# Optimization experiments

Measured on AMD Instinct MI355X. Metric: run time of the kernel, lower is better.

The kernel has to match this reference:

```python
import jax, jax.numpy as jnp
import numpy as np

N = 10000      # nodes
E = 160000     # edges (avg degree 16)
H = 128        # hidden_dim
L = 4          # propagation_depth
G = 64         # graphs in batch
ATOM_V = 119
BOND_V = 5
AVG_D_LOG = 1.0
EPS_SCALE = 1e-8


def setup_inputs() -> dict:
    key = jax.random.key(0)
    ks = jax.random.split(key, 12)
    x = jax.random.randint(ks[0], (N,), 0, ATOM_V)
    edge_index = jax.random.randint(ks[1], (2, E), 0, N)
    edge_attr = jax.random.randint(ks[2], (E,), 0, BOND_V)
    batch = jnp.sort(jax.random.randint(ks[3], (N,), 0, G))
    atom_emb = jax.random.normal(ks[4], (ATOM_V, H), jnp.float32) * 0.1
    bond_emb = jax.random.normal(ks[5], (BOND_V, H), jnp.float32) * 0.1
    pre_W = jax.random.normal(ks[6], (L, 3 * H, H), jnp.float32) / np.sqrt(3 * H)
    pre_b = jnp.zeros((L, H), jnp.float32)
    post_W = jax.random.normal(ks[7], (L, 10 * H, H), jnp.float32) / np.sqrt(10 * H)
    post_b = jnp.zeros((L, H), jnp.float32)
    out_W1 = jax.random.normal(ks[8], (3 * H, H), jnp.float32) / np.sqrt(3 * H)
    out_b1 = jnp.zeros((H,), jnp.float32)
    out_W2 = jax.random.normal(ks[9], (H, 1), jnp.float32) / np.sqrt(H)
    out_b2 = jnp.zeros((1,), jnp.float32)
    return {"x": x, "edge_index": edge_index, "edge_attr": edge_attr, "batch": batch,
            "atom_emb": atom_emb, "bond_emb": bond_emb,
            "pre_W": pre_W, "pre_b": pre_b, "post_W": post_W, "post_b": post_b,
            "out_W1": out_W1, "out_b1": out_b1, "out_W2": out_W2, "out_b2": out_b2}


def _seg_mean_sum_max(v, idx, num_seg, cnt):
    s = jax.ops.segment_sum(v, idx, num_segments=num_seg)
    mean = s / jnp.maximum(cnt, 1.0)[:, None]
    mx = jax.ops.segment_max(v, idx, num_segments=num_seg)
    mx = jnp.where(cnt[:, None] > 0, mx, 0.0)  # empty segments -> 0 (torch scatter)
    return mean, s, mx


def _clean(a):
    return jnp.where(jnp.isnan(a) | jnp.isinf(a), 0.0, a)


def reference(x, edge_index, edge_attr, batch, atom_emb, bond_emb,
              pre_W, pre_b, post_W, post_b, out_W1, out_b1, out_W2, out_b2):
    h = atom_emb[x]            # [N, H] atom encoder
    e = bond_emb[edge_attr]    # [E, H] bond encoder
    row, col = edge_index[0], edge_index[1]
    n = h.shape[0]
    deg = jax.ops.segment_sum(jnp.ones_like(col, jnp.float32), col, num_segments=n)
    D = deg[:, None]
    logD = jnp.log(D + 1.0)
    amp_fac = logD / AVG_D_LOG                       # amplification scaler
    att_fac = AVG_D_LOG / jnp.maximum(logD, EPS_SCALE)  # attenuation scaler
    n_layers = pre_W.shape[0]
    for l in range(n_layers):
        h_in = h
        z2 = jnp.concatenate([h[row], h[col], e], axis=-1)         # [E, 3H]
        msg = z2 @ pre_W[l] + pre_b[l]                             # pretrans (1 layer, no act)
        mean, s, mx = _seg_mean_sum_max(msg, col, n, deg)
        hagg = jnp.concatenate([mean, s, mx], axis=-1)             # [N, 3H]
        hcat = jnp.concatenate([hagg, hagg * amp_fac, hagg * att_fac, h_in], axis=-1)  # [N, 10H]
        h = hcat @ post_W[l] + post_b[l]                           # posttrans (1 layer)
        h = h + h_in                                               # residual
    # readout over graphs
    cnt = jax.ops.segment_sum(jnp.ones((n,), jnp.float32), batch, num_segments=G)
    rmean, rsum, rmax = _seg_mean_sum_max(h, batch, G, cnt)
    r = _clean(jnp.concatenate([rmean, rsum, rmax], axis=-1))      # [G, 3H]
    out = jax.nn.relu(r @ out_W1 + out_b1) @ out_W2 + out_b2       # [G, 1]
    return _clean(out)
```

## Files before the change

kernel.cpp:

```cpp
#include <hip/hip_runtime.h>
#include <hip/hip_bf16.h>
#include <math.h>

#define NN 10000
#define NE 160000
#define HD 128
#define NL 4
#define NG 64

typedef __attribute__((ext_vector_type(8))) short bf16x8;
typedef __attribute__((ext_vector_type(4))) short bf16x4;
typedef __attribute__((ext_vector_type(4))) float f32x4;

static __device__ __forceinline__ short f2bf(float f) {
    unsigned u = __float_as_uint(f);
    unsigned r = (u + 0x7FFFu + ((u >> 16) & 1u)) >> 16;
    return (short)r;
}
static __device__ __forceinline__ float bf2f(short s) {
    return __uint_as_float(((unsigned)(unsigned short)s) << 16);
}

__global__ void setup1_kernel(const int* __restrict__ x, const float* __restrict__ atom_emb,
                              float* __restrict__ h, float* __restrict__ deg,
                              int* __restrict__ cursor) {
    int idx = blockIdx.x * 256 + threadIdx.x;
    if (idx < NN) { deg[idx] = 0.f; cursor[idx] = 0; }
    if (idx < NN * HD) {
        int n = idx >> 7, f = idx & 127;
        h[idx] = atom_emb[x[n] * HD + f];
    }
}

__global__ __launch_bounds__(256) void setup2_kernel(
    const int* __restrict__ col, float* __restrict__ deg,
    const float* __restrict__ bond_emb,
    const float* __restrict__ pre_W, const float* __restrict__ pre_b,
    const float* __restrict__ post_W,
    float* __restrict__ btab, short* __restrict__ pre_Wt, short* __restrict__ post_Wt) {
    int b = blockIdx.x;
    if (b < 625) {
        int e = b * 256 + threadIdx.x;
        if (e < NE) atomicAdd(&deg[col[e]], 1.f);
        return;
    }
    if (b < 645) {
        int lb = b - 625;
        if (threadIdx.x < 128) {
            int l = lb / 5, bb = lb % 5;
            int f = threadIdx.x;
            const float* W2 = pre_W + (size_t)l * 384 * HD + 256 * HD;
            const float* eb = bond_emb + bb * HD;
            float acc = pre_b[l * HD + f];
            for (int k = 0; k < HD; ++k) acc = fmaf(eb[k], W2[k * HD + f], acc);
            btab[(l * 5 + bb) * HD + f] = acc;
        }
        return;
    }
    int idx = (b - 645) * 256 + threadIdx.x;
    if (idx < NL * 4 * 256 * 32) {
        int l = idx >> 15;
        int r = idx & 32767;
        int kblk = r >> 13;
        int rr = r & 8191;
        int j = rr >> 5, k = rr & 31;
        const float* Wl = pre_W + (size_t)l * 384 * HD;
        float v = (j < 128) ? Wl[(kblk * 32 + k) * HD + j]
                            : Wl[(128 + kblk * 32 + k) * HD + (j - 128)];
        pre_Wt[idx] = f2bf(v);
    }
    if (idx < NL * 40 * 128 * 32) {
        int l = idx / 163840;
        int r = idx % 163840;
        int kblk = r >> 12;
        int rr = r & 4095;
        int j = rr >> 5, k = rr & 31;
        post_Wt[idx] = f2bf(post_W[(size_t)l * 163840 + (size_t)(kblk * 32 + k) * HD + j]);
    }
}

__global__ __launch_bounds__(1024) void scan_facs_kernel(const float* __restrict__ deg,
                                                         int* __restrict__ offsets,
                                                         float* __restrict__ amp,
                                                         float* __restrict__ att) {
    __shared__ int s[1024];
    int t = threadIdx.x;
    int base = t * 10;
    int v[10];
    int lsum = 0;
    #pragma unroll
    for (int i = 0; i < 10; ++i) {
        int idx = base + i;
        int d = (idx < NN) ? (int)deg[idx] : 0;
        v[i] = d;
        lsum += d;
        if (idx < NN) {
            float logD = logf((float)d + 1.f);
            amp[idx] = logD;
            att[idx] = 1.f / fmaxf(logD, 1e-8f);
        }
    }
    s[t] = lsum;
    __syncthreads();
    for (int off = 1; off < 1024; off <<= 1) {
        int x2 = (t >= off) ? s[t - off] : 0;
        __syncthreads();
        s[t] += x2;
        __syncthreads();
    }
    int run = s[t] - lsum;
    #pragma unroll
    for (int i = 0; i < 10; ++i) {
        int idx = base + i;
        if (idx < NN) offsets[idx] = run;
        run += v[i];
    }
    if (t == 1023) offsets[NN] = run;
}

__global__ void scatter_kernel(const int* __restrict__ row, const int* __restrict__ col,
                               const int* __restrict__ ea, const int* __restrict__ offsets,
                               int* __restrict__ cursor, int* __restrict__ perm) {
    int e = blockIdx.x * 256 + threadIdx.x;
    if (e < NE) {
        int c = col[e];
        int pos = offsets[c] + atomicAdd(&cursor[c], 1);
        perm[pos] = row[e] | (ea[e] << 14);
    }
}

__global__ __launch_bounds__(256) void pre_gemm_mfma(const float* __restrict__ h,
                                                     const short* __restrict__ Wt,
                                                     short* __restrict__ hw0,
                                                     float* __restrict__ hw1) {
    __shared__ short Ap[16][136];
    int t = threadIdx.x;
    int nb = blockIdx.x * 16;
    {
        int nl = t >> 4, f = (t & 15) * 8;
        int n = nb + nl;
        const float* src = h + (size_t)n * HD + f;
        float4 x0 = *(const float4*)src, x1 = *(const float4*)(src + 4);
        bf16x8 pk;
        pk[0]=f2bf(x0.x); pk[1]=f2bf(x0.y); pk[2]=f2bf(x0.z); pk[3]=f2bf(x0.w);
        pk[4]=f2bf(x1.x); pk[5]=f2bf(x1.y); pk[6]=f2bf(x1.z); pk[7]=f2bf(x1.w);
        *(bf16x8*)&Ap[nl][f] = pk;
    }
    __syncthreads();
    int wave = t >> 6, lane = t & 63;
    int lx = lane & 15, kb = lane >> 4;
    f32x4 acc[4];
    #pragma unroll
    for (int j = 0; j < 4; ++j) acc[j] = (f32x4){0.f, 0.f, 0.f, 0.f};

    for (int ks = 0; ks < 4; ++ks) {
        bf16x8 a = *(const bf16x8*)&Ap[lx][ks * 32 + kb * 8];
        const short* bp = Wt + (size_t)ks * 8192 + (size_t)(wave * 64 + lx) * 32 + kb * 8;
        #pragma unroll
        for (int jj = 0; jj < 4; ++jj) {
            bf16x8 bfr = *(const bf16x8*)(bp + jj * 512);
            acc[jj] = __builtin_amdgcn_mfma_f32_16x16x32_bf16(a, bfr, acc[jj], 0, 0, 0);
        }
    }
    #pragma unroll
    for (int jj = 0; jj < 4; ++jj) {
        int c = wave * 64 + jj * 16 + lx;
        #pragma unroll
        for (int r_ = 0; r_ < 4; ++r_) {
            int n2 = nb + kb * 4 + r_;
            if (c < 128) hw0[(size_t)n2 * HD + c] = f2bf(acc[jj][r_]);
            else         hw1[(size_t)n2 * HD + (c - 128)] = acc[jj][r_];
        }
    }
}

__global__ __launch_bounds__(256) void agg_node_gemm_mfma(
    const short* __restrict__ hw0, const float* __restrict__ hw1,
    const float* __restrict__ btab,
    const int* __restrict__ offsets, const int* __restrict__ perm,
    const float* __restrict__ hin,
    const float* __restrict__ amp, const float* __restrict__ att,
    const short* __restrict__ Wt , const float* __restrict__ bias,
    float* __restrict__ hout,
    const short* __restrict__ nextWt ,
    short* __restrict__ hw0n, float* __restrict__ hw1n) {
    __shared__ short Ap[16][1288];
    __shared__ short Ap2[16][136];
    __shared__ float btab_s[5][128];
    int t = threadIdx.x;
    int nb = blockIdx.x * 16;

    if (t < 160) {
        int b = t >> 5, f4 = (t & 31) * 4;
        *(f32x4*)&btab_s[b][f4] = *(const f32x4*)(btab + b * HD + f4);
    }
    __syncthreads();

    {
        int nl = t >> 4;
        int n = nb + nl;
        int f = (t & 15) * 8;
        int s0 = offsets[n];
        int d = offsets[n + 1] - s0;
        f32x4 sum0 = {0.f,0.f,0.f,0.f}, sum1 = {0.f,0.f,0.f,0.f};
        f32x4 mx0 = {-INFINITY,-INFINITY,-INFINITY,-INFINITY};
        f32x4 mx1 = mx0;
        int i = 0;
        for (; i + 2 <= d; i += 2) {
            int p0 = perm[s0 + i], p1 = perm[s0 + i + 1];
            bf16x8 a0 = *(const bf16x8*)(hw0 + (size_t)(p0 & 16383) * HD + f);
            bf16x8 a1 = *(const bf16x8*)(hw0 + (size_t)(p1 & 16383) * HD + f);
            const float* t0 = &btab_s[p0 >> 14][f];
            const float* t1 = &btab_s[p1 >> 14][f];
            f32x4 b00 = *(const f32x4*)t0, b01 = *(const f32x4*)(t0 + 4);
            f32x4 b10 = *(const f32x4*)t1, b11 = *(const f32x4*)(t1 + 4);
            f32x4 v00, v01, v10, v11;
            #pragma unroll
            for (int q = 0; q < 4; ++q) {
                v00[q] = bf2f(a0[q]) + b00[q];
                v01[q] = bf2f(a0[q + 4]) + b01[q];
                v10[q] = bf2f(a1[q]) + b10[q];
                v11[q] = bf2f(a1[q + 4]) + b11[q];
            }
            sum0 += v00 + v10; sum1 += v01 + v11;
            #pragma unroll
            for (int q = 0; q < 4; ++q) {
                mx0[q] = fmaxf(mx0[q], fmaxf(v00[q], v10[q]));
                mx1[q] = fmaxf(mx1[q], fmaxf(v01[q], v11[q]));
            }
        }
        if (i < d) {
            int p0 = perm[s0 + i];
            bf16x8 a0 = *(const bf16x8*)(hw0 + (size_t)(p0 & 16383) * HD + f);
            const float* t0 = &btab_s[p0 >> 14][f];
            f32x4 b00 = *(const f32x4*)t0, b01 = *(const f32x4*)(t0 + 4);
            f32x4 v00, v01;
            #pragma unroll
            for (int q = 0; q < 4; ++q) {
                v00[q] = bf2f(a0[q]) + b00[q];
                v01[q] = bf2f(a0[q + 4]) + b01[q];
            }
            sum0 += v00; sum1 += v01;
            #pragma unroll
            for (int q = 0; q < 4; ++q) {
                mx0[q] = fmaxf(mx0[q], v00[q]);
                mx1[q] = fmaxf(mx1[q], v01[q]);
            }
        }
        const float* cp = hw1 + (size_t)n * HD + f;
        f32x4 c0 = *(const f32x4*)cp, c1 = *(const f32x4*)(cp + 4);
        f32x4 me0, me1, so0, so1, mo0, mo1;
        if (d > 0) {
            float df = (float)d, di = 1.f / df;
            so0 = sum0 + df * c0;  so1 = sum1 + df * c1;
            me0 = sum0 * di + c0;  me1 = sum1 * di + c1;
            mo0 = mx0 + c0;        mo1 = mx1 + c1;
        } else {
            me0 = (f32x4){0.f,0.f,0.f,0.f}; me1 = me0;
            so0 = me0; so1 = me0; mo0 = me0; mo1 = me0;
        }
        float f_amp = amp[n], f_att = att[n];
        #pragma unroll
        for (int fi = 0; fi < 3; ++fi) {
            float fac = (fi == 0) ? 1.f : ((fi == 1) ? f_amp : f_att);
            #pragma unroll
            for (int ag = 0; ag < 3; ++ag) {
                f32x4 r0 = (ag == 0) ? me0 : ((ag == 1) ? so0 : mo0);
                f32x4 r1 = (ag == 0) ? me1 : ((ag == 1) ? so1 : mo1);
                bf16x8 pk;
                #pragma unroll
                for (int q = 0; q < 4; ++q) {
                    pk[q]     = f2bf(r0[q] * fac);
                    pk[q + 4] = f2bf(r1[q] * fac);
                }
                *(bf16x8*)&Ap[nl][(fi * 3 + ag) * 128 + f] = pk;
            }
        }
        {
            const float* src = hin + (size_t)n * HD + f;
            float4 x0 = *(const float4*)src, x1 = *(const float4*)(src + 4);
            bf16x8 pk;
            pk[0]=f2bf(x0.x); pk[1]=f2bf(x0.y); pk[2]=f2bf(x0.z); pk[3]=f2bf(x0.w);
            pk[4]=f2bf(x1.x); pk[5]=f2bf(x1.y); pk[6]=f2bf(x1.z); pk[7]=f2bf(x1.w);
            *(bf16x8*)&Ap[nl][9 * 128 + f] = pk;
        }
    }
    __syncthreads();

    int wave = t >> 6, lane = t & 63;
    int lx = lane & 15, kb = lane >> 4;
    f32x4 acc0 = {0.f,0.f,0.f,0.f}, acc1 = acc0;
    for (int ks = 0; ks < 40; ++ks) {
        bf16x8 a = *(const bf16x8*)&Ap[lx][ks * 32 + kb * 8];
        const short* bp = Wt + (size_t)ks * 4096 + (size_t)(wave * 32 + lx) * 32 + kb * 8;
        bf16x8 b0 = *(const bf16x8*)bp;
        bf16x8 b1 = *(const bf16x8*)(bp + 512);
        acc0 = __builtin_amdgcn_mfma_f32_16x16x32_bf16(a, b0, acc0, 0, 0, 0);
        acc1 = __builtin_amdgcn_mfma_f32_16x16x32_bf16(a, b1, acc1, 0, 0, 0);
    }
    #pragma unroll
    for (int jj = 0; jj < 2; ++jj) {
        int c = wave * 32 + jj * 16 + lx;
        float bc = bias[c];
        f32x4 av = jj ? acc1 : acc0;
        #pragma unroll
        for (int r_ = 0; r_ < 4; ++r_) {
            int n2 = nb + kb * 4 + r_;
            size_t off = (size_t)n2 * HD + c;
            float ho = av[r_] + bc + hin[off];
            hout[off] = ho;
            Ap2[n2 - nb][c] = f2bf(ho);
        }
    }
    if (nextWt == nullptr) return;
    __syncthreads();

    f32x4 acc[4];
    #pragma unroll
    for (int j = 0; j < 4; ++j) acc[j] = (f32x4){0.f, 0.f, 0.f, 0.f};
    for (int ks = 0; ks < 4; ++ks) {
        bf16x8 a = *(const bf16x8*)&Ap2[lx][ks * 32 + kb * 8];
        const short* bp = nextWt + (size_t)ks * 8192 + (size_t)(wave * 64 + lx) * 32 + kb * 8;
        #pragma unroll
        for (int jj = 0; jj < 4; ++jj) {
            bf16x8 bfr = *(const bf16x8*)(bp + jj * 512);
            acc[jj] = __builtin_amdgcn_mfma_f32_16x16x32_bf16(a, bfr, acc[jj], 0, 0, 0);
        }
    }
    #pragma unroll
    for (int jj = 0; jj < 4; ++jj) {
        int c = wave * 64 + jj * 16 + lx;
        #pragma unroll
        for (int r_ = 0; r_ < 4; ++r_) {
            int n2 = nb + kb * 4 + r_;
            if (c < 128) hw0n[(size_t)n2 * HD + c] = f2bf(acc[jj][r_]);
            else         hw1n[(size_t)n2 * HD + (c - 128)] = acc[jj][r_];
        }
    }
}

__global__ __launch_bounds__(256) void pool_out_kernel(
    const float* __restrict__ h, const int* __restrict__ batch,
    const float* __restrict__ W1, const float* __restrict__ b1,
    const float* __restrict__ W2, const float* __restrict__ b2,
    float* __restrict__ out)
{
    __shared__ float rs[384];
    __shared__ float red[256];
    __shared__ float s2[128], m2[128];
    int g = blockIdx.x, t = threadIdx.x;
    int lo = 0, hi = NN;
    while (lo < hi) { int mid = (lo + hi) >> 1; if (batch[mid] < g) lo = mid + 1; else hi = mid; }
    int lo2 = lo, hi2 = NN;
    while (lo2 < hi2) { int mid = (lo2 + hi2) >> 1; if (batch[mid] < g + 1) lo2 = mid + 1; else hi2 = mid; }
    int cnt = lo2 - lo;
    int f = t & 127, grp = t >> 7;
    float sum = 0.f, mx = -INFINITY;
    for (int n = lo + grp; n < lo2; n += 2) {
        float v = h[(size_t)n * HD + f];
        sum += v; mx = fmaxf(mx, v);
    }
    if (grp == 1) { s2[f] = sum; m2[f] = mx; }
    __syncthreads();
    if (grp == 0) {
        sum += s2[f]; mx = fmaxf(mx, m2[f]);
        float mean = (cnt > 0) ? sum / (float)cnt : 0.f;
        float so = (cnt > 0) ? sum : 0.f;
        float mo = (cnt > 0) ? mx : 0.f;
        if (isnan(mean) || isinf(mean)) mean = 0.f;
        if (isnan(so) || isinf(so)) so = 0.f;
        if (isnan(mo) || isinf(mo)) mo = 0.f;
        rs[f] = mean; rs[128 + f] = so; rs[256 + f] = mo;
    }
    __syncthreads();
    {
        int j = t & 127, kh = t >> 7;
        float acc = 0.f;
        for (int k = kh * 192; k < kh * 192 + 192; ++k)
            acc = fmaf(rs[k], W1[k * HD + j], acc);
        red[t] = acc;
    }
    __syncthreads();
    if (t < 128) {
        float v = fmaxf(red[t] + red[128 + t] + b1[t], 0.f);
        red[t] = v * W2[t];
    }
    __syncthreads();
    for (int s = 64; s > 0; s >>= 1) {
        if (t < s) red[t] += red[t + s];
        __syncthreads();
    }
    if (t == 0) {
        float o = red[0] + b2[0];
        if (isnan(o) || isinf(o)) o = 0.f;
        out[g] = o;
    }
}

extern "C" void kernel_launch(void* const* d_in, const int* in_sizes, int n_in,
                              void* d_out, int out_size, void* d_ws, size_t ws_size,
                              hipStream_t stream)
{
    const int* x          = (const int*)d_in[0];
    const int* ei         = (const int*)d_in[1];
    const int* ea         = (const int*)d_in[2];
    const int* batch      = (const int*)d_in[3];
    const float* atom_emb = (const float*)d_in[4];
    const float* bond_emb = (const float*)d_in[5];
    const float* pre_W    = (const float*)d_in[6];
    const float* pre_b    = (const float*)d_in[7];
    const float* post_W   = (const float*)d_in[8];
    const float* post_b   = (const float*)d_in[9];
    const float* out_W1   = (const float*)d_in[10];
    const float* out_b1   = (const float*)d_in[11];
    const float* out_W2   = (const float*)d_in[12];
    const float* out_b2   = (const float*)d_in[13];
    float* out = (float*)d_out;
    const int* row = ei;
    const int* col = ei + NE;

    char* p = (char*)d_ws;
    auto alloc = [&](size_t bytes) { char* r = p; p += (bytes + 255) & ~(size_t)255; return r; };
    float*    deg     = (float*)alloc((size_t)NN * 4);
    float*    amp     = (float*)alloc((size_t)NN * 4);
    float*    att     = (float*)alloc((size_t)NN * 4);
    int*      offsets = (int*)alloc((size_t)(NN + 1) * 4);
    int*      cursor  = (int*)alloc((size_t)NN * 4);
    int*      perm    = (int*)alloc((size_t)NE * 4);
    float*    hA      = (float*)alloc((size_t)NN * HD * 4);
    float*    hB      = (float*)alloc((size_t)NN * HD * 4);
    short*    hw0A    = (short*)alloc((size_t)NN * HD * 2);
    short*    hw0B    = (short*)alloc((size_t)NN * HD * 2);
    float*    hw1A    = (float*)alloc((size_t)NN * HD * 4);
    float*    hw1B    = (float*)alloc((size_t)NN * HD * 4);
    float*    btab    = (float*)alloc((size_t)NL * 5 * HD * 4);
    short*    pre_Wt  = (short*)alloc((size_t)NL * 4 * 256 * 32 * 2);
    short*    post_Wt = (short*)alloc((size_t)NL * 40 * 128 * 32 * 2);

    setup1_kernel<<<(NN * HD) / 256, 256, 0, stream>>>(x, atom_emb, hA, deg, cursor);
    setup2_kernel<<<645 + (NL * 40 * 128 * 32 + 255) / 256, 256, 0, stream>>>(
        col, deg, bond_emb, pre_W, pre_b, post_W, btab, pre_Wt, post_Wt);
    scan_facs_kernel<<<1, 1024, 0, stream>>>(deg, offsets, amp, att);
    scatter_kernel<<<(NE + 255) / 256, 256, 0, stream>>>(row, col, ea, offsets, cursor, perm);

    pre_gemm_mfma<<<NN / 16, 256, 0, stream>>>(hA, pre_Wt, hw0A, hw1A);

    float* curH = hA;
    float* nxtH = hB;
    for (int l = 0; l < NL; ++l) {
        short* hw0_in  = (l & 1) ? hw0B : hw0A;
        float* hw1_in  = (l & 1) ? hw1B : hw1A;
        short* hw0_out = (l & 1) ? hw0A : hw0B;
        float* hw1_out = (l & 1) ? hw1A : hw1B;
        const short* nextWt = (l + 1 < NL) ? (pre_Wt + (size_t)(l + 1) * 4 * 256 * 32) : nullptr;
        agg_node_gemm_mfma<<<NN / 16, 256, 0, stream>>>(
            hw0_in, hw1_in, btab + (size_t)l * 5 * HD, offsets, perm,
            curH, amp, att, post_Wt + (size_t)l * 40 * 128 * 32,
            post_b + (size_t)l * HD, nxtH, nextWt, hw0_out, hw1_out);
        float* tmp = curH; curH = nxtH; nxtH = tmp;
    }

    pool_out_kernel<<<NG, 256, 0, stream>>>(curH, batch, out_W1, out_b1, out_W2, out_b2, out);
}
```

Baseline: 287.5 us.

## Fuse all stages into one cooperative persistent kernel with grid syncs

Replaces the chain of separate kernel launches (setup, scan, scatter, pre-GEMM, four layer kernels, pooling) with one cooperative kernel of 625 blocks that separates stages with grid.sync, removing per-launch overhead and inter-kernel gaps. The layer kernel also shrinks its shared-memory A tile by storing only the three aggregates in bf16 and applying the amp/att scalers and the h_in conversion on the fly during the MFMA loop, which lowers LDS use to allow more resident blocks. The degree scan now runs in a single 256-thread block inside the grid, and grid-wide barriers add their own sync cost. A multi-kernel fallback is kept when cooperative occupancy is insufficient.

```diff
diff --git a/kernel.cpp b/kernel.cpp
--- a/kernel.cpp
+++ b/kernel.cpp
@@ -1,12 +1,19 @@
 #include <hip/hip_runtime.h>
+#include <hip/hip_cooperative_groups.h>
 #include <hip/hip_bf16.h>
 #include <math.h>
+
+namespace cg = cooperative_groups;
 
 #define NN 10000
 #define NE 160000
 #define HD 128
 #define NL 4
 #define NG 64
+#define NBLK 625
+#define NTHR 256
+#define GRIDTHREADS 160000
+#define SMEM_BYTES 19584
 
 typedef __attribute__((ext_vector_type(8))) short bf16x8;
 typedef __attribute__((ext_vector_type(4))) short bf16x4;
@@ -20,6 +27,272 @@
 static __device__ __forceinline__ float bf2f(short s) {
     return __uint_as_float(((unsigned)(unsigned short)s) << 16);
 }
+
+
+__device__ __forceinline__ void pre_gemm_body(char* smem, int t, int nb,
+        const float* __restrict__ h, const short* __restrict__ Wt,
+        short* __restrict__ hw0, float* __restrict__ hw1) {
+    short (*Ap)[136] = (short(*)[136])smem;
+    {
+        int nl = t >> 4, f = (t & 15) * 8;
+        int n = nb + nl;
+        const float* src = h + (size_t)n * HD + f;
+        float4 x0 = *(const float4*)src, x1 = *(const float4*)(src + 4);
+        bf16x8 pk;
+        pk[0]=f2bf(x0.x); pk[1]=f2bf(x0.y); pk[2]=f2bf(x0.z); pk[3]=f2bf(x0.w);
+        pk[4]=f2bf(x1.x); pk[5]=f2bf(x1.y); pk[6]=f2bf(x1.z); pk[7]=f2bf(x1.w);
+        *(bf16x8*)&Ap[nl][f] = pk;
+    }
+    __syncthreads();
+    int wave = t >> 6, lane = t & 63;
+    int lx = lane & 15, kb = lane >> 4;
+    f32x4 acc[4];
+    #pragma unroll
+    for (int j = 0; j < 4; ++j) acc[j] = (f32x4){0.f, 0.f, 0.f, 0.f};
+    for (int ks = 0; ks < 4; ++ks) {
+        bf16x8 a = *(const bf16x8*)&Ap[lx][ks * 32 + kb * 8];
+        const short* bp = Wt + (size_t)ks * 8192 + (size_t)(wave * 64 + lx) * 32 + kb * 8;
+        #pragma unroll
+        for (int jj = 0; jj < 4; ++jj) {
+            bf16x8 bfr = *(const bf16x8*)(bp + jj * 512);
+            acc[jj] = __builtin_amdgcn_mfma_f32_16x16x32_bf16(a, bfr, acc[jj], 0, 0, 0);
+        }
+    }
+    #pragma unroll
+    for (int jj = 0; jj < 4; ++jj) {
+        int c = wave * 64 + jj * 16 + lx;
+        #pragma unroll
+        for (int r_ = 0; r_ < 4; ++r_) {
+            int n2 = nb + kb * 4 + r_;
+            if (c < 128) hw0[(size_t)n2 * HD + c] = f2bf(acc[jj][r_]);
+            else         hw1[(size_t)n2 * HD + (c - 128)] = acc[jj][r_];
+        }
+    }
+}
+
+__device__ __forceinline__ void fused_layer_body(char* smem, int t, int nb,
+        const short* __restrict__ hw0_in, const float* __restrict__ hw1_in,
+        const float* __restrict__ btabL,
+        const int* __restrict__ offsets, const int* __restrict__ perm,
+        const float* __restrict__ curH,
+        const float* __restrict__ amp, const float* __restrict__ att,
+        const short* __restrict__ Wt , const float* __restrict__ bias,
+        float* __restrict__ nxtH,
+        const short* __restrict__ nextWt, short* __restrict__ hw0o, float* __restrict__ hw1o) {
+    short (*aggB)[3][132] = (short(*)[3][132])smem;
+    float (*btab_s)[128]  = (float(*)[128])(smem + 12672);
+    short (*Ap2)[136]     = (short(*)[136])(smem + 15232);
+
+    if (t < 160) {
+        int bb = t >> 5, f4 = (t & 31) * 4;
+        *(f32x4*)&btab_s[bb][f4] = *(const f32x4*)(btabL + bb * HD + f4);
+    }
+    __syncthreads();
+
+    {
+        int nl = t >> 4;
+        int n = nb + nl;
+        int f = (t & 15) * 8;
+        int s0 = offsets[n];
+        int d = offsets[n + 1] - s0;
+        f32x4 sum0 = {0.f,0.f,0.f,0.f}, sum1 = {0.f,0.f,0.f,0.f};
+        f32x4 mx0 = {-INFINITY,-INFINITY,-INFINITY,-INFINITY};
+        f32x4 mx1 = mx0;
+        int i = 0;
+        for (; i + 2 <= d; i += 2) {
+            int p0 = perm[s0 + i], p1 = perm[s0 + i + 1];
+            bf16x8 a0 = *(const bf16x8*)(hw0_in + (size_t)(p0 & 16383) * HD + f);
+            bf16x8 a1 = *(const bf16x8*)(hw0_in + (size_t)(p1 & 16383) * HD + f);
+            const float* t0 = &btab_s[p0 >> 14][f];
+            const float* t1 = &btab_s[p1 >> 14][f];
+            f32x4 b00 = *(const f32x4*)t0, b01 = *(const f32x4*)(t0 + 4);
+            f32x4 b10 = *(const f32x4*)t1, b11 = *(const f32x4*)(t1 + 4);
+            f32x4 v00, v01, v10, v11;
+            #pragma unroll
+            for (int q = 0; q < 4; ++q) {
+                v00[q] = bf2f(a0[q]) + b00[q];
+                v01[q] = bf2f(a0[q + 4]) + b01[q];
+                v10[q] = bf2f(a1[q]) + b10[q];
+                v11[q] = bf2f(a1[q + 4]) + b11[q];
+            }
+            sum0 += v00 + v10; sum1 += v01 + v11;
+            #pragma unroll
+            for (int q = 0; q < 4; ++q) {
+                mx0[q] = fmaxf(mx0[q], fmaxf(v00[q], v10[q]));
+                mx1[q] = fmaxf(mx1[q], fmaxf(v01[q], v11[q]));
+            }
+        }
+        if (i < d) {
+            int p0 = perm[s0 + i];
+            bf16x8 a0 = *(const bf16x8*)(hw0_in + (size_t)(p0 & 16383) * HD + f);
+            const float* t0 = &btab_s[p0 >> 14][f];
+            f32x4 b00 = *(const f32x4*)t0, b01 = *(const f32x4*)(t0 + 4);
+            f32x4 v00, v01;
+            #pragma unroll
+            for (int q = 0; q < 4; ++q) {
+                v00[q] = bf2f(a0[q]) + b00[q];
+                v01[q] = bf2f(a0[q + 4]) + b01[q];
+            }
+            sum0 += v00; sum1 += v01;
+            #pragma unroll
+            for (int q = 0; q < 4; ++q) {
+                mx0[q] = fmaxf(mx0[q], v00[q]);
+                mx1[q] = fmaxf(mx1[q], v01[q]);
+            }
+        }
+        const float* cp = hw1_in + (size_t)n * HD + f;
+        f32x4 c0 = *(const f32x4*)cp, c1 = *(const f32x4*)(cp + 4);
+        f32x4 me0, me1, so0, so1, mo0, mo1;
+        if (d > 0) {
+            float df = (float)d, di = 1.f / df;
+            so0 = sum0 + df * c0;  so1 = sum1 + df * c1;
+            me0 = sum0 * di + c0;  me1 = sum1 * di + c1;
+            mo0 = mx0 + c0;        mo1 = mx1 + c1;
+        } else {
+            me0 = (f32x4){0.f,0.f,0.f,0.f}; me1 = me0;
+            so0 = me0; so1 = me0; mo0 = me0; mo1 = me0;
+        }
+        bf16x8 pk;
+        #pragma unroll
+        for (int q = 0; q < 4; ++q) { pk[q] = f2bf(me0[q]); pk[q+4] = f2bf(me1[q]); }
+        *(bf16x8*)&aggB[nl][0][f] = pk;
+        #pragma unroll
+        for (int q = 0; q < 4; ++q) { pk[q] = f2bf(so0[q]); pk[q+4] = f2bf(so1[q]); }
+        *(bf16x8*)&aggB[nl][1][f] = pk;
+        #pragma unroll
+        for (int q = 0; q < 4; ++q) { pk[q] = f2bf(mo0[q]); pk[q+4] = f2bf(mo1[q]); }
+        *(bf16x8*)&aggB[nl][2][f] = pk;
+    }
+    __syncthreads();
+
+    int wave = t >> 6, lane = t & 63;
+    int lx = lane & 15, kb = lane >> 4;
+    int n_lx = nb + lx;
+    float famp = amp[n_lx], fatt = att[n_lx];
+    f32x4 acc0 = {0.f,0.f,0.f,0.f}, acc1 = acc0;
+    for (int ks = 0; ks < 40; ++ks) {
+        int r = ks >> 2;
+        int kk = (ks & 3) * 32 + kb * 8;
+        bf16x8 afrag;
+        if (r < 9) {
+            int ag = r % 3, fi = r / 3;
+            bf16x8 raw = *(const bf16x8*)&aggB[lx][ag][kk];
+            if (fi == 0) afrag = raw;
+            else {
+                float fac = (fi == 1) ? famp : fatt;
+                #pragma unroll
+                for (int q = 0; q < 8; ++q) afrag[q] = f2bf(bf2f(raw[q]) * fac);
+            }
+        } else {
+            const float* src = curH + (size_t)n_lx * HD + kk;
+            float4 x0 = *(const float4*)src, x1 = *(const float4*)(src + 4);
+            afrag[0]=f2bf(x0.x); afrag[1]=f2bf(x0.y); afrag[2]=f2bf(x0.z); afrag[3]=f2bf(x0.w);
+            afrag[4]=f2bf(x1.x); afrag[5]=f2bf(x1.y); afrag[6]=f2bf(x1.z); afrag[7]=f2bf(x1.w);
+        }
+        const short* bp = Wt + (size_t)ks * 4096 + (size_t)(wave * 32 + lx) * 32 + kb * 8;
+        bf16x8 b0 = *(const bf16x8*)bp;
+        bf16x8 b1 = *(const bf16x8*)(bp + 512);
+        acc0 = __builtin_amdgcn_mfma_f32_16x16x32_bf16(afrag, b0, acc0, 0, 0, 0);
+        acc1 = __builtin_amdgcn_mfma_f32_16x16x32_bf16(afrag, b1, acc1, 0, 0, 0);
+    }
+    #pragma unroll
+    for (int jj = 0; jj < 2; ++jj) {
+        int c = wave * 32 + jj * 16 + lx;
+        float bc = bias[c];
+        f32x4 av = jj ? acc1 : acc0;
+        #pragma unroll
+        for (int r_ = 0; r_ < 4; ++r_) {
+            int n2 = nb + kb * 4 + r_;
+            size_t off = (size_t)n2 * HD + c;
+            float ho = av[r_] + bc + curH[off];
+            nxtH[off] = ho;
+            Ap2[n2 - nb][c] = f2bf(ho);
+        }
+    }
+    if (nextWt != nullptr) {
+        __syncthreads();
+        f32x4 acc[4];
+        #pragma unroll
+        for (int j = 0; j < 4; ++j) acc[j] = (f32x4){0.f, 0.f, 0.f, 0.f};
+        for (int ks = 0; ks < 4; ++ks) {
+            bf16x8 aa = *(const bf16x8*)&Ap2[lx][ks * 32 + kb * 8];
+            const short* bp = nextWt + (size_t)ks * 8192 + (size_t)(wave * 64 + lx) * 32 + kb * 8;
+            #pragma unroll
+            for (int jj = 0; jj < 4; ++jj) {
+                bf16x8 bfr = *(const bf16x8*)(bp + jj * 512);
+                acc[jj] = __builtin_amdgcn_mfma_f32_16x16x32_bf16(aa, bfr, acc[jj], 0, 0, 0);
+            }
+        }
+        #pragma unroll
+        for (int jj = 0; jj < 4; ++jj) {
+            int c = wave * 64 + jj * 16 + lx;
+            #pragma unroll
+            for (int r_ = 0; r_ < 4; ++r_) {
+                int n2 = nb + kb * 4 + r_;
+                if (c < 128) hw0o[(size_t)n2 * HD + c] = f2bf(acc[jj][r_]);
+                else         hw1o[(size_t)n2 * HD + (c - 128)] = acc[jj][r_];
+            }
+        }
+    }
+}
+
+__device__ __forceinline__ void pool_body(char* smem, int t, int g,
+        const float* __restrict__ h, const int* __restrict__ batch,
+        const float* __restrict__ W1, const float* __restrict__ b1,
+        const float* __restrict__ W2, const float* __restrict__ b2,
+        float* __restrict__ out) {
+    float* rs  = (float*)smem;
+    float* red = rs + 384;
+    float* s2  = red + 256;
+    float* m2  = s2 + 128;
+    int lo = 0, hi = NN;
+    while (lo < hi) { int mid = (lo + hi) >> 1; if (batch[mid] < g) lo = mid + 1; else hi = mid; }
+    int lo2 = lo, hi2 = NN;
+    while (lo2 < hi2) { int mid = (lo2 + hi2) >> 1; if (batch[mid] < g + 1) lo2 = mid + 1; else hi2 = mid; }
+    int cnt = lo2 - lo;
+    int f = t & 127, grp = t >> 7;
+    float sum = 0.f, mx = -INFINITY;
+    for (int n = lo + grp; n < lo2; n += 2) {
+        float v = h[(size_t)n * HD + f];
+        sum += v; mx = fmaxf(mx, v);
+    }
+    if (grp == 1) { s2[f] = sum; m2[f] = mx; }
+    __syncthreads();
+    if (grp == 0) {
+        sum += s2[f]; mx = fmaxf(mx, m2[f]);
+        float mean = (cnt > 0) ? sum / (float)cnt : 0.f;
+        float so = (cnt > 0) ? sum : 0.f;
+        float mo = (cnt > 0) ? mx : 0.f;
+        if (isnan(mean) || isinf(mean)) mean = 0.f;
+        if (isnan(so) || isinf(so)) so = 0.f;
+        if (isnan(mo) || isinf(mo)) mo = 0.f;
+        rs[f] = mean; rs[128 + f] = so; rs[256 + f] = mo;
+    }
+    __syncthreads();
+    {
+        int j = t & 127, kh = t >> 7;
+        float acc = 0.f;
+        for (int k = kh * 192; k < kh * 192 + 192; ++k)
+            acc = fmaf(rs[k], W1[k * HD + j], acc);
+        red[t] = acc;
+    }
+    __syncthreads();
+    if (t < 128) {
+        float v = fmaxf(red[t] + red[128 + t] + b1[t], 0.f);
+        red[t] = v * W2[t];
+    }
+    __syncthreads();
+    for (int s = 64; s > 0; s >>= 1) {
+        if (t < s) red[t] += red[t + s];
+        __syncthreads();
+    }
+    if (t == 0) {
+        float o = red[0] + b2[0];
+        if (isnan(o) || isinf(o)) o = 0.f;
+        out[g] = o;
+    }
+}
+
 
 __global__ void setup1_kernel(const int* __restrict__ x, const float* __restrict__ atom_emb,
                               float* __restrict__ h, float* __restrict__ deg,
@@ -129,273 +402,153 @@
     }
 }
 
-__global__ __launch_bounds__(256) void pre_gemm_mfma(const float* __restrict__ h,
-                                                     const short* __restrict__ Wt,
-                                                     short* __restrict__ hw0,
-                                                     float* __restrict__ hw1) {
-    __shared__ short Ap[16][136];
-    int t = threadIdx.x;
-    int nb = blockIdx.x * 16;
+__global__ __launch_bounds__(256, 4) void pre_gemm_kernel(const float* __restrict__ h,
+                                                          const short* __restrict__ Wt,
+                                                          short* __restrict__ hw0,
+                                                          float* __restrict__ hw1) {
+    __shared__ __align__(16) char smem[4352];
+    pre_gemm_body(smem, threadIdx.x, blockIdx.x * 16, h, Wt, hw0, hw1);
+}
+
+__global__ __launch_bounds__(256, 4) void fused_kernel(
+    const short* hw0_in, const float* hw1_in, const float* btabL,
+    const int* offsets, const int* perm, const float* curH,
+    const float* amp, const float* att,
+    const short* Wt, const float* bias, float* nxtH,
+    const short* nextWt, short* hw0o, float* hw1o) {
+    __shared__ __align__(16) char smem[SMEM_BYTES];
+    fused_layer_body(smem, threadIdx.x, blockIdx.x * 16, hw0_in, hw1_in, btabL,
+                     offsets, perm, curH, amp, att, Wt, bias, nxtH, nextWt, hw0o, hw1o);
+}
+
+__global__ __launch_bounds__(256) void pool_out_kernel(
+    const float* h, const int* batch,
+    const float* W1, const float* b1, const float* W2, const float* b2,
+    float* out) {
+    __shared__ __align__(16) char smem[3584];
+    pool_body(smem, threadIdx.x, blockIdx.x, h, batch, W1, b1, W2, b2, out);
+}
+
+
+struct MegaArgs {
+    const int* x; const int* row; const int* col; const int* ea; const int* batch;
+    const float* atom_emb; const float* bond_emb;
+    const float* pre_W; const float* pre_b; const float* post_W; const float* post_b;
+    const float* out_W1; const float* out_b1; const float* out_W2; const float* out_b2;
+    float* out;
+    float* deg; float* amp; float* att; int* offsets; int* cursor; int* perm;
+    float* hA; float* hB; short* hw0A; short* hw0B; float* hw1A; float* hw1B;
+    float* btab; short* pre_Wt; short* post_Wt;
+};
+
+__global__ __launch_bounds__(256, 4) void mega_kernel(MegaArgs a) {
+    cg::grid_group grid = cg::this_grid();
+    __shared__ __align__(16) char smem[SMEM_BYTES];
+    int t = threadIdx.x, b = blockIdx.x;
+    int gid = b * NTHR + t;
+    int nb = b * 16;
+
+    #pragma unroll
+    for (int i = 0; i < 8; ++i) {
+        int idx = gid + i * GRIDTHREADS;
+        int n = idx >> 7, f = idx & 127;
+        a.hA[idx] = a.atom_emb[a.x[n] * HD + f];
+    }
+    if (gid < NN) { a.deg[gid] = 0.f; a.cursor[gid] = 0; }
+    if (gid < NL * 4 * 256 * 32) {
+        int idx = gid;
+        int l = idx >> 15;
+        int r = idx & 32767;
+        int kblk = r >> 13;
+        int rr = r & 8191;
+        int j = rr >> 5, k = rr & 31;
+        const float* Wl = a.pre_W + (size_t)l * 384 * HD;
+        float v = (j < 128) ? Wl[(kblk * 32 + k) * HD + j]
+                            : Wl[(128 + kblk * 32 + k) * HD + (j - 128)];
+        a.pre_Wt[idx] = f2bf(v);
+    }
+    for (int idx = gid; idx < NL * 40 * 128 * 32; idx += GRIDTHREADS) {
+        int l = idx / 163840;
+        int r = idx % 163840;
+        int kblk = r >> 12;
+        int rr = r & 4095;
+        int j = rr >> 5, k = rr & 31;
+        a.post_Wt[idx] = f2bf(a.post_W[(size_t)l * 163840 + (size_t)(kblk * 32 + k) * HD + j]);
+    }
+    if (b < 20 && t < 128) {
+        int l = b / 5, bb = b % 5;
+        const float* W2 = a.pre_W + (size_t)l * 384 * HD + 256 * HD;
+        const float* eb = a.bond_emb + bb * HD;
+        float acc = a.pre_b[l * HD + t];
+        for (int k = 0; k < HD; ++k) acc = fmaf(eb[k], W2[k * HD + t], acc);
+        a.btab[(l * 5 + bb) * HD + t] = acc;
+    }
+    grid.sync();
+
+    atomicAdd(&a.deg[a.col[gid]], 1.f);
+    grid.sync();
+
+    if (gid < NN) {
+        float logD = logf(a.deg[gid] + 1.f);
+        a.amp[gid] = logD;
+        a.att[gid] = 1.f / fmaxf(logD, 1e-8f);
+    }
+    if (b == 0) {
+        int* ssc = (int*)smem;
+        int lsum = 0;
+        for (int i = 0; i < 40; ++i) {
+            int idx = t * 40 + i;
+            lsum += (idx < NN) ? (int)a.deg[idx] : 0;
+        }
+        ssc[t] = lsum;
+        __syncthreads();
+        for (int off = 1; off < 256; off <<= 1) {
+            int x2 = (t >= off) ? ssc[t - off] : 0;
+            __syncthreads();
+            ssc[t] += x2;
+            __syncthreads();
+        }
+        int run = ssc[t] - lsum;
+        for (int i = 0; i < 40; ++i) {
+            int idx = t * 40 + i;
+            if (idx < NN) { a.offsets[idx] = run; run += (int)a.deg[idx]; }
+        }
+        if (t == 255) a.offsets[NN] = run;
+    }
+    grid.sync();
+
     {
-        int nl = t >> 4, f = (t & 15) * 8;
-        int n = nb + nl;
-        const float* src = h + (size_t)n * HD + f;
-        float4 x0 = *(const float4*)src, x1 = *(const float4*)(src + 4);
-        bf16x8 pk;
-        pk[0]=f2bf(x0.x); pk[1]=f2bf(x0.y); pk[2]=f2bf(x0.z); pk[3]=f2bf(x0.w);
-        pk[4]=f2bf(x1.x); pk[5]=f2bf(x1.y); pk[6]=f2bf(x1.z); pk[7]=f2bf(x1.w);
-        *(bf16x8*)&Ap[nl][f] = pk;
-    }
-    __syncthreads();
-    int wave = t >> 6, lane = t & 63;
-    int lx = lane & 15, kb = lane >> 4;
-    f32x4 acc[4];
-    #pragma unroll
-    for (int j = 0; j < 4; ++j) acc[j] = (f32x4){0.f, 0.f, 0.f, 0.f};
-
-    for (int ks = 0; ks < 4; ++ks) {
-        bf16x8 a = *(const bf16x8*)&Ap[lx][ks * 32 + kb * 8];
-        const short* bp = Wt + (size_t)ks * 8192 + (size_t)(wave * 64 + lx) * 32 + kb * 8;
-        #pragma unroll
-        for (int jj = 0; jj < 4; ++jj) {
-            bf16x8 bfr = *(const bf16x8*)(bp + jj * 512);
-            acc[jj] = __builtin_amdgcn_mfma_f32_16x16x32_bf16(a, bfr, acc[jj], 0, 0, 0);
-        }
-    }
-    #pragma unroll
-    for (int jj = 0; jj < 4; ++jj) {
-        int c = wave * 64 + jj * 16 + lx;
-        #pragma unroll
-        for (int r_ = 0; r_ < 4; ++r_) {
-            int n2 = nb + kb * 4 + r_;
-            if (c < 128) hw0[(size_t)n2 * HD + c] = f2bf(acc[jj][r_]);
-            else         hw1[(size_t)n2 * HD + (c - 128)] = acc[jj][r_];
-        }
-    }
-}
-
-__global__ __launch_bounds__(256) void agg_node_gemm_mfma(
-    const short* __restrict__ hw0, const float* __restrict__ hw1,
-    const float* __restrict__ btab,
-    const int* __restrict__ offsets, const int* __restrict__ perm,
-    const float* __restrict__ hin,
-    const float* __restrict__ amp, const float* __restrict__ att,
-    const short* __restrict__ Wt , const float* __restrict__ bias,
-    float* __restrict__ hout,
-    const short* __restrict__ nextWt ,
-    short* __restrict__ hw0n, float* __restrict__ hw1n) {
-    __shared__ short Ap[16][1288];
-    __shared__ short Ap2[16][136];
-    __shared__ float btab_s[5][128];
-    int t = threadIdx.x;
-    int nb = blockIdx.x * 16;
-
-    if (t < 160) {
-        int b = t >> 5, f4 = (t & 31) * 4;
-        *(f32x4*)&btab_s[b][f4] = *(const f32x4*)(btab + b * HD + f4);
-    }
-    __syncthreads();
-
-    {
-        int nl = t >> 4;
-        int n = nb + nl;
-        int f = (t & 15) * 8;
-        int s0 = offsets[n];
-        int d = offsets[n + 1] - s0;
-        f32x4 sum0 = {0.f,0.f,0.f,0.f}, sum1 = {0.f,0.f,0.f,0.f};
-        f32x4 mx0 = {-INFINITY,-INFINITY,-INFINITY,-INFINITY};
-        f32x4 mx1 = mx0;
-        int i = 0;
-        for (; i + 2 <= d; i += 2) {
-            int p0 = perm[s0 + i], p1 = perm[s0 + i + 1];
-            bf16x8 a0 = *(const bf16x8*)(hw0 + (size_t)(p0 & 16383) * HD + f);
-            bf16x8 a1 = *(const bf16x8*)(hw0 + (size_t)(p1 & 16383) * HD + f);
-            const float* t0 = &btab_s[p0 >> 14][f];
-            const float* t1 = &btab_s[p1 >> 14][f];
-            f32x4 b00 = *(const f32x4*)t0, b01 = *(const f32x4*)(t0 + 4);
-            f32x4 b10 = *(const f32x4*)t1, b11 = *(const f32x4*)(t1 + 4);
-            f32x4 v00, v01, v10, v11;
-            #pragma unroll
-            for (int q = 0; q < 4; ++q) {
-                v00[q] = bf2f(a0[q]) + b00[q];
-                v01[q] = bf2f(a0[q + 4]) + b01[q];
-                v10[q] = bf2f(a1[q]) + b10[q];
-                v11[q] = bf2f(a1[q + 4]) + b11[q];
-            }
-            sum0 += v00 + v10; sum1 += v01 + v11;
-            #pragma unroll
-            for (int q = 0; q < 4; ++q) {
-                mx0[q] = fmaxf(mx0[q], fmaxf(v00[q], v10[q]));
-                mx1[q] = fmaxf(mx1[q], fmaxf(v01[q], v11[q]));
-            }
-        }
-        if (i < d) {
-            int p0 = perm[s0 + i];
-            bf16x8 a0 = *(const bf16x8*)(hw0 + (size_t)(p0 & 16383) * HD + f);
-            const float* t0 = &btab_s[p0 >> 14][f];
-            f32x4 b00 = *(const f32x4*)t0, b01 = *(const f32x4*)(t0 + 4);
-            f32x4 v00, v01;
-            #pragma unroll
-            for (int q = 0; q < 4; ++q) {
-                v00[q] = bf2f(a0[q]) + b00[q];
-                v01[q] = bf2f(a0[q + 4]) + b01[q];
-            }
-            sum0 += v00; sum1 += v01;
-            #pragma unroll
-            for (int q = 0; q < 4; ++q) {
-                mx0[q] = fmaxf(mx0[q], v00[q]);
-                mx1[q] = fmaxf(mx1[q], v01[q]);
-            }
-        }
-        const float* cp = hw1 + (size_t)n * HD + f;
-        f32x4 c0 = *(const f32x4*)cp, c1 = *(const f32x4*)(cp + 4);
-        f32x4 me0, me1, so0, so1, mo0, mo1;
-        if (d > 0) {
-            float df = (float)d, di = 1.f / df;
-            so0 = sum0 + df * c0;  so1 = sum1 + df * c1;
-            me0 = sum0 * di + c0;  me1 = sum1 * di + c1;
-            mo0 = mx0 + c0;        mo1 = mx1 + c1;
-        } else {
-            me0 = (f32x4){0.f,0.f,0.f,0.f}; me1 = me0;
-            so0 = me0; so1 = me0; mo0 = me0; mo1 = me0;
-        }
-        float f_amp = amp[n], f_att = att[n];
-        #pragma unroll
-        for (int fi = 0; fi < 3; ++fi) {
-            float fac = (fi == 0) ? 1.f : ((fi == 1) ? f_amp : f_att);
-            #pragma unroll
-            for (int ag = 0; ag < 3; ++ag) {
-                f32x4 r0 = (ag == 0) ? me0 : ((ag == 1) ? so0 : mo0);
-                f32x4 r1 = (ag == 0) ? me1 : ((ag == 1) ? so1 : mo1);
-                bf16x8 pk;
-                #pragma unroll
-                for (int q = 0; q < 4; ++q) {
-                    pk[q]     = f2bf(r0[q] * fac);
-                    pk[q + 4] = f2bf(r1[q] * fac);
-                }
-                *(bf16x8*)&Ap[nl][(fi * 3 + ag) * 128 + f] = pk;
-            }
-        }
-        {
-            const float* src = hin + (size_t)n * HD + f;
-            float4 x0 = *(const float4*)src, x1 = *(const float4*)(src + 4);
-            bf16x8 pk;
-            pk[0]=f2bf(x0.x); pk[1]=f2bf(x0.y); pk[2]=f2bf(x0.z); pk[3]=f2bf(x0.w);
-            pk[4]=f2bf(x1.x); pk[5]=f2bf(x1.y); pk[6]=f2bf(x1.z); pk[7]=f2bf(x1.w);
-            *(bf16x8*)&Ap[nl][9 * 128 + f] = pk;
-        }
-    }
-    __syncthreads();
-
-    int wave = t >> 6, lane = t & 63;
-    int lx = lane & 15, kb = lane >> 4;
-    f32x4 acc0 = {0.f,0.f,0.f,0.f}, acc1 = acc0;
-    for (int ks = 0; ks < 40; ++ks) {
-        bf16x8 a = *(const bf16x8*)&Ap[lx][ks * 32 + kb * 8];
-        const short* bp = Wt + (size_t)ks * 4096 + (size_t)(wave * 32 + lx) * 32 + kb * 8;
-        bf16x8 b0 = *(const bf16x8*)bp;
-        bf16x8 b1 = *(const bf16x8*)(bp + 512);
-        acc0 = __builtin_amdgcn_mfma_f32_16x16x32_bf16(a, b0, acc0, 0, 0, 0);
-        acc1 = __builtin_amdgcn_mfma_f32_16x16x32_bf16(a, b1, acc1, 0, 0, 0);
-    }
-    #pragma unroll
-    for (int jj = 0; jj < 2; ++jj) {
-        int c = wave * 32 + jj * 16 + lx;
-        float bc = bias[c];
-        f32x4 av = jj ? acc1 : acc0;
-        #pragma unroll
-        for (int r_ = 0; r_ < 4; ++r_) {
-            int n2 = nb + kb * 4 + r_;
-            size_t off = (size_t)n2 * HD + c;
-            float ho = av[r_] + bc + hin[off];
-            hout[off] = ho;
-            Ap2[n2 - nb][c] = f2bf(ho);
-        }
-    }
-    if (nextWt == nullptr) return;
-    __syncthreads();
-
-    f32x4 acc[4];
-    #pragma unroll
-    for (int j = 0; j < 4; ++j) acc[j] = (f32x4){0.f, 0.f, 0.f, 0.f};
-    for (int ks = 0; ks < 4; ++ks) {
-        bf16x8 a = *(const bf16x8*)&Ap2[lx][ks * 32 + kb * 8];
-        const short* bp = nextWt + (size_t)ks * 8192 + (size_t)(wave * 64 + lx) * 32 + kb * 8;
-        #pragma unroll
-        for (int jj = 0; jj < 4; ++jj) {
-            bf16x8 bfr = *(const bf16x8*)(bp + jj * 512);
-            acc[jj] = __builtin_amdgcn_mfma_f32_16x16x32_bf16(a, bfr, acc[jj], 0, 0, 0);
-        }
-    }
-    #pragma unroll
-    for (int jj = 0; jj < 4; ++jj) {
-        int c = wave * 64 + jj * 16 + lx;
-        #pragma unroll
-        for (int r_ = 0; r_ < 4; ++r_) {
-            int n2 = nb + kb * 4 + r_;
-            if (c < 128) hw0n[(size_t)n2 * HD + c] = f2bf(acc[jj][r_]);
-            else         hw1n[(size_t)n2 * HD + (c - 128)] = acc[jj][r_];
-        }
-    }
-}
-
-__global__ __launch_bounds__(256) void pool_out_kernel(
-    const float* __restrict__ h, const int* __restrict__ batch,
-    const float* __restrict__ W1, const float* __restrict__ b1,
-    const float* __restrict__ W2, const float* __restrict__ b2,
-    float* __restrict__ out)
-{
-    __shared__ float rs[384];
-    __shared__ float red[256];
-    __shared__ float s2[128], m2[128];
-    int g = blockIdx.x, t = threadIdx.x;
-    int lo = 0, hi = NN;
-    while (lo < hi) { int mid = (lo + hi) >> 1; if (batch[mid] < g) lo = mid + 1; else hi = mid; }
-    int lo2 = lo, hi2 = NN;
-    while (lo2 < hi2) { int mid = (lo2 + hi2) >> 1; if (batch[mid] < g + 1) lo2 = mid + 1; else hi2 = mid; }
-    int cnt = lo2 - lo;
-    int f = t & 127, grp = t >> 7;
-    float sum = 0.f, mx = -INFINITY;
-    for (int n = lo + grp; n < lo2; n += 2) {
-        float v = h[(size_t)n * HD + f];
-        sum += v; mx = fmaxf(mx, v);
-    }
-    if (grp == 1) { s2[f] = sum; m2[f] = mx; }
-    __syncthreads();
-    if (grp == 0) {
-        sum += s2[f]; mx = fmaxf(mx, m2[f]);
-        float mean = (cnt > 0) ? sum / (float)cnt : 0.f;
-        float so = (cnt > 0) ? sum : 0.f;
-        float mo = (cnt > 0) ? mx : 0.f;
-        if (isnan(mean) || isinf(mean)) mean = 0.f;
-        if (isnan(so) || isinf(so)) so = 0.f;
-        if (isnan(mo) || isinf(mo)) mo = 0.f;
-        rs[f] = mean; rs[128 + f] = so; rs[256 + f] = mo;
-    }
-    __syncthreads();
-    {
-        int j = t & 127, kh = t >> 7;
-        float acc = 0.f;
-        for (int k = kh * 192; k < kh * 192 + 192; ++k)
-            acc = fmaf(rs[k], W1[k * HD + j], acc);
-        red[t] = acc;
-    }
-    __syncthreads();
-    if (t < 128) {
-        float v = fmaxf(red[t] + red[128 + t] + b1[t], 0.f);
-        red[t] = v * W2[t];
-    }
-    __syncthreads();
-    for (int s = 64; s > 0; s >>= 1) {
-        if (t < s) red[t] += red[t + s];
-        __syncthreads();
-    }
-    if (t == 0) {
-        float o = red[0] + b2[0];
-        if (isnan(o) || isinf(o)) o = 0.f;
-        out[g] = o;
-    }
-}
+        int c = a.col[gid];
+        int pos = a.offsets[c] + atomicAdd(&a.cursor[c], 1);
+        a.perm[pos] = a.row[gid] | (a.ea[gid] << 14);
+    }
+    grid.sync();
+
+    pre_gemm_body(smem, t, nb, a.hA, a.pre_Wt, a.hw0A, a.hw1A);
+    grid.sync();
+
+    float* curH = a.hA;
+    float* nxtH = a.hB;
+    const short* hw0_in = a.hw0A;
+    const float* hw1_in = a.hw1A;
+    for (int l = 0; l < NL; ++l) {
+        short* hw0_out = (l & 1) ? a.hw0A : a.hw0B;
+        float* hw1_out = (l & 1) ? a.hw1A : a.hw1B;
+        const short* nextWt = (l + 1 < NL) ? (a.pre_Wt + (size_t)(l + 1) * 32768) : nullptr;
+        fused_layer_body(smem, t, nb, hw0_in, hw1_in, a.btab + (size_t)l * 5 * HD,
+                         a.offsets, a.perm, curH, a.amp, a.att,
+                         a.post_Wt + (size_t)l * 163840, a.post_b + (size_t)l * HD,
+                         nxtH, nextWt, hw0_out, hw1_out);
+        float* tmp = curH; curH = nxtH; nxtH = tmp;
+        hw0_in = hw0_out; hw1_in = hw1_out;
+        grid.sync();
+    }
+
+    if (b < NG) {
+        pool_body(smem, t, b, curH, a.batch, a.out_W1, a.out_b1, a.out_W2, a.out_b2, a.out);
+    }
+}
+
 
 extern "C" void kernel_launch(void* const* d_in, const int* in_sizes, int n_in,
                               void* d_out, int out_size, void* d_ws, size_t ws_size,
@@ -437,27 +590,51 @@
     short*    pre_Wt  = (short*)alloc((size_t)NL * 4 * 256 * 32 * 2);
     short*    post_Wt = (short*)alloc((size_t)NL * 40 * 128 * 32 * 2);
 
+    int occ = 0;
+    hipError_t oerr = hipOccupancyMaxActiveBlocksPerMultiprocessor(&occ, mega_kernel, NTHR, 0);
+    int dev = 0, numCU = 0;
+    hipGetDevice(&dev);
+    hipDeviceGetAttribute(&numCU, hipDeviceAttributeMultiprocessorCount, dev);
+    bool use_coop = (oerr == hipSuccess) && (occ > 0) && ((long)occ * (long)numCU >= NBLK);
+
+    if (use_coop) {
+        MegaArgs ma;
+        ma.x = x; ma.row = row; ma.col = col; ma.ea = ea; ma.batch = batch;
+        ma.atom_emb = atom_emb; ma.bond_emb = bond_emb;
+        ma.pre_W = pre_W; ma.pre_b = pre_b; ma.post_W = post_W; ma.post_b = post_b;
+        ma.out_W1 = out_W1; ma.out_b1 = out_b1; ma.out_W2 = out_W2; ma.out_b2 = out_b2;
+        ma.out = out;
+        ma.deg = deg; ma.amp = amp; ma.att = att; ma.offsets = offsets; ma.cursor = cursor;
+        ma.perm = perm; ma.hA = hA; ma.hB = hB;
+        ma.hw0A = hw0A; ma.hw0B = hw0B; ma.hw1A = hw1A; ma.hw1B = hw1B;
+        ma.btab = btab; ma.pre_Wt = pre_Wt; ma.post_Wt = post_Wt;
+        void* kargs[] = { (void*)&ma };
+        hipLaunchCooperativeKernel((const void*)mega_kernel, dim3(NBLK), dim3(NTHR),
+                                   kargs, 0, stream);
+        return;
+    }
+
     setup1_kernel<<<(NN * HD) / 256, 256, 0, stream>>>(x, atom_emb, hA, deg, cursor);
     setup2_kernel<<<645 + (NL * 40 * 128 * 32 + 255) / 256, 256, 0, stream>>>(
         col, deg, bond_emb, pre_W, pre_b, post_W, btab, pre_Wt, post_Wt);
     scan_facs_kernel<<<1, 1024, 0, stream>>>(deg, offsets, amp, att);
     scatter_kernel<<<(NE + 255) / 256, 256, 0, stream>>>(row, col, ea, offsets, cursor, perm);
-
-    pre_gemm_mfma<<<NN / 16, 256, 0, stream>>>(hA, pre_Wt, hw0A, hw1A);
+    pre_gemm_kernel<<<NBLK, 256, 0, stream>>>(hA, pre_Wt, hw0A, hw1A);
 
     float* curH = hA;
     float* nxtH = hB;
+    const short* hw0_in = hw0A;
+    const float* hw1_in = hw1A;
     for (int l = 0; l < NL; ++l) {
-        short* hw0_in  = (l & 1) ? hw0B : hw0A;
-        float* hw1_in  = (l & 1) ? hw1B : hw1A;
         short* hw0_out = (l & 1) ? hw0A : hw0B;
         float* hw1_out = (l & 1) ? hw1A : hw1B;
-        const short* nextWt = (l + 1 < NL) ? (pre_Wt + (size_t)(l + 1) * 4 * 256 * 32) : nullptr;
-        agg_node_gemm_mfma<<<NN / 16, 256, 0, stream>>>(
+        const short* nextWt = (l + 1 < NL) ? (pre_Wt + (size_t)(l + 1) * 32768) : nullptr;
+        fused_kernel<<<NBLK, 256, 0, stream>>>(
             hw0_in, hw1_in, btab + (size_t)l * 5 * HD, offsets, perm,
-            curH, amp, att, post_Wt + (size_t)l * 40 * 128 * 32,
+            curH, amp, att, post_Wt + (size_t)l * 163840,
             post_b + (size_t)l * HD, nxtH, nextWt, hw0_out, hw1_out);
         float* tmp = curH; curH = nxtH; nxtH = tmp;
+        hw0_in = hw0_out; hw1_in = hw1_out;
     }
 
     pool_out_kernel<<<NG, 256, 0, stream>>>(curH, batch, out_W1, out_b1, out_W2, out_b2, out);
```

After: 310.4 us. 1.08x slower.
